# Kernel optimization log

Hardware: AMD Instinct MI355X
Metric: run time of the kernel (lower is better)

Reference implementation:

```python
import jax, jax.numpy as jnp
import numpy as np

NITERS = 5  # mean-field iterations (niters in __init__)


def setup_inputs() -> dict:
    key = jax.random.key(0)
    k1, k2 = jax.random.split(key)
    B, L, C, H, W = 2, 21, 3, 96, 96
    E0 = jax.random.normal(k1, (B, L, H, W), dtype=jnp.float32)
    Refs = jax.random.normal(k2, (B, C, H, W), dtype=jnp.float32)
    # potts_init: weight = ones(L,L) - eye(L)
    Mu_W = jnp.ones((L, L), dtype=jnp.float32) - jnp.eye(L, dtype=jnp.float32)
    return {"E0": E0, "Refs": Refs, "Mu_W": Mu_W}


def _affinity(Refs):
    # Reference-guided dense adjacency (BatchedAdjacency): row-normalized
    # Gaussian affinity on guide features, one N x N matrix per batch element.
    B, C, H, W = Refs.shape
    N = H * W
    f = Refs.reshape(B, C, N).transpose(0, 2, 1)  # [B, N, C]
    sq = jnp.sum(f * f, axis=-1)  # [B, N]
    D = sq[:, :, None] + sq[:, None, :] - 2.0 * jnp.einsum('bnc,bmc->bnm', f, f)
    A = jnp.exp(-0.5 * D)  # [B, N, N]
    return A / jnp.sum(A, axis=-1, keepdims=True)


def reference(E0, Refs, Mu_W):
    B, L, H, W = E0.shape
    N = H * W
    A = _affinity(Refs)  # computed once, reused every iteration
    E0f = E0.reshape(B, L, N)
    Qf = jax.nn.softmax(-E0f, axis=1)  # Q = softmax(-E0, dim=1)
    for _ in range(NITERS):
        # Potts compatibility transform (channel mixing): Mu(Q)
        M = jnp.einsum('kl,bln->bkn', Mu_W, Qf)
        # adjacency message passing: W(Mu(Q), Refs)
        msg = jnp.einsum('bnm,blm->bln', A, M)
        Qf = jax.nn.softmax(-(E0f + msg), axis=1)
    return Qf.reshape(B, L, H, W)
```

## Files before the change

### kernel.cpp

```cpp
#include <hip/hip_runtime.h>
#include <hip/hip_bf16.h>


#define BB 2
#define LL 21
#define LP (LL + 1)
#define NNPX 9216
#define NITERS 5
#define LOG2E 1.4426950408889634f

typedef __attribute__((ext_vector_type(8))) short short8;
typedef __attribute__((ext_vector_type(4))) float f32x4;

static __device__ inline unsigned int pk_bf16(float a, float b) {
    __hip_bfloat162 h = __float22bfloat162_rn(make_float2(a, b));
    unsigned int u;
    __builtin_memcpy(&u, &h, 4);
    return u;
}

__global__ __launch_bounds__(256) void k_prep(
        const float* __restrict__ E0, const float* __restrict__ Refs,
        const float* __restrict__ Mu,
        float4* __restrict__ FN, float4* __restrict__ FS,
        __hip_bfloat16* __restrict__ MQ) {
    __shared__ float muS[LL * LL];
    for (int i = threadIdx.x; i < LL * LL; i += 256) muS[i] = Mu[i];
    __syncthreads();

    int idx = blockIdx.x * 256 + threadIdx.x;
    int b = idx / NNPX, n = idx % NNPX;

    const float* rb = Refs + (size_t)b * 3 * NNPX + n;
    float r0 = rb[0], r1 = rb[NNPX], r2 = rb[2 * NNPX];
    FN[idx] = make_float4(r0, r1, r2, 0.f);
    float g = -0.5f * (r0 * r0 + r1 * r1 + r2 * r2);
    FS[idx] = make_float4(g * LOG2E, r0 * LOG2E, r1 * LOG2E, r2 * LOG2E);

    const float* eb = E0 + (size_t)b * LL * NNPX + n;
    float x[LL];
    float mx = -1e30f;
    for (int l = 0; l < LL; ++l) { x[l] = -eb[(size_t)l * NNPX]; mx = fmaxf(mx, x[l]); }
    float s = 0.f;
    for (int l = 0; l < LL; ++l) { x[l] = __builtin_amdgcn_exp2f((x[l] - mx) * LOG2E); s += x[l]; }
    float rs = __builtin_amdgcn_rcpf(s);
    for (int l = 0; l < LL; ++l) x[l] *= rs;

    __hip_bfloat16* mq = MQ + (size_t)b * LL * NNPX + n;
    for (int k = 0; k < LL; ++k) {
        float a = 0.f;
        for (int l = 0; l < LL; ++l) a += muS[k * LL + l] * x[l];
        mq[(size_t)k * NNPX] = __float2bfloat16(a);
    }
}

__global__ __launch_bounds__(256) void k_accum(
        const float4* __restrict__ FS, const float4* __restrict__ FN,
        const unsigned int* __restrict__ MQbf, float* __restrict__ Ppart, int S) {
    __shared__ __align__(16) unsigned short Wlds[64 * 72];
    __shared__ __align__(16) unsigned short Mlds[32 * 72];

    int t = threadIdx.x;
    int rb = blockIdx.x;
    int s  = blockIdx.y;
    int b  = rb / 144;
    int n0 = (rb % 144) * 64;
    int wv = t >> 6, lane = t & 63;

    for (int i = t; i < 32 * 72 / 2; i += 256) ((unsigned int*)Mlds)[i] = 0;
    if (t < 32) ((unsigned int*)&Mlds[21 * 72])[t] = 0x3F803F80u;

    int mq = t & 15;
    int ng = t >> 4;
    float4 fnr[4];
    for (int i = 0; i < 4; ++i) fnr[i] = FN[b * NNPX + n0 + ng + 16 * i];

    f32x4 acc0 = {0.f, 0.f, 0.f, 0.f};
    f32x4 acc1 = {0.f, 0.f, 0.f, 0.f};

    const unsigned int* mqb = MQbf + (size_t)b * LL * (NNPX / 2);

    for (int tile = s; tile < 144; tile += S) {
        int m0 = tile * 64;
        float4 fsr[4];
        for (int j = 0; j < 4; ++j) fsr[j] = FS[b * NNPX + m0 + 4 * mq + j];

        __syncthreads();

        for (int e = t; e < 21 * 32; e += 256) {
            int l = e >> 5, mo = e & 31;
            ((unsigned int*)&Mlds[l * 72])[mo] = mqb[(size_t)l * (NNPX / 2) + m0 / 2 + mo];
        }
        for (int i = 0; i < 4; ++i) {
            float4 f = fnr[i];
            float w0 = __builtin_amdgcn_exp2f(fsr[0].x + f.x * fsr[0].y + f.y * fsr[0].z + f.z * fsr[0].w);
            float w1 = __builtin_amdgcn_exp2f(fsr[1].x + f.x * fsr[1].y + f.y * fsr[1].z + f.z * fsr[1].w);
            float w2 = __builtin_amdgcn_exp2f(fsr[2].x + f.x * fsr[2].y + f.y * fsr[2].z + f.z * fsr[2].w);
            float w3 = __builtin_amdgcn_exp2f(fsr[3].x + f.x * fsr[3].y + f.y * fsr[3].z + f.z * fsr[3].w);
            uint2 pk;
            pk.x = pk_bf16(w0, w1);
            pk.y = pk_bf16(w2, w3);
            int n = ng + 16 * i;
            *(uint2*)&Wlds[n * 72 + 4 * mq] = pk;
        }
        __syncthreads();

        int row = wv * 16 + (lane & 15);
        int kof = (lane >> 4) * 8;
        short8 a0 = *(const short8*)&Wlds[row * 72 + kof];
        short8 a1 = *(const short8*)&Wlds[row * 72 + kof + 32];
        short8 b00 = *(const short8*)&Mlds[(lane & 15) * 72 + kof];
        short8 b01 = *(const short8*)&Mlds[(lane & 15) * 72 + kof + 32];
        short8 b10 = *(const short8*)&Mlds[(16 + (lane & 15)) * 72 + kof];
        short8 b11 = *(const short8*)&Mlds[(16 + (lane & 15)) * 72 + kof + 32];
        acc0 = __builtin_amdgcn_mfma_f32_16x16x32_bf16(a0, b00, acc0, 0, 0, 0);
        acc0 = __builtin_amdgcn_mfma_f32_16x16x32_bf16(a1, b01, acc0, 0, 0, 0);
        acc1 = __builtin_amdgcn_mfma_f32_16x16x32_bf16(a0, b10, acc1, 0, 0, 0);
        acc1 = __builtin_amdgcn_mfma_f32_16x16x32_bf16(a1, b11, acc1, 0, 0, 0);
    }

    int col = lane & 15, qr = lane >> 4;
    float* pp = Ppart + ((size_t)(s * BB + b) * LP) * NNPX;
    for (int r = 0; r < 4; ++r) {
        int n = n0 + wv * 16 + qr * 4 + r;
        pp[(size_t)col * NNPX + n] = acc0[r];
        if (col < LP - 16) pp[(size_t)(16 + col) * NNPX + n] = acc1[r];
    }
}

template <bool LAST>
__global__ __launch_bounds__(256) void k_softmax(
        const float* __restrict__ E0, const float* __restrict__ Ppart,
        const float* __restrict__ Mu,
        __hip_bfloat16* __restrict__ MQ, float* __restrict__ Out, int S) {
    __shared__ float muS[LL * LL];
    for (int i = threadIdx.x; i < LL * LL; i += 256) muS[i] = Mu[i];
    __syncthreads();

    int idx = blockIdx.x * 256 + threadIdx.x;
    int b = idx / NNPX, n = idx % NNPX;

    float P[LP];
    for (int l = 0; l < LP; ++l) P[l] = 0.f;
    for (int s = 0; s < S; ++s) {
        const float* pp = Ppart + ((size_t)(s * BB + b) * LP) * NNPX + n;
        for (int l = 0; l < LP; ++l) P[l] += pp[(size_t)l * NNPX];
    }
    float rinv = __builtin_amdgcn_rcpf(P[LL]);

    const float* eb = E0 + (size_t)b * LL * NNPX + n;
    float mx = -1e30f;
    for (int l = 0; l < LL; ++l) {
        P[l] = -(eb[(size_t)l * NNPX] + P[l] * rinv);
        mx = fmaxf(mx, P[l]);
    }
    float ssum = 0.f;
    for (int l = 0; l < LL; ++l) { P[l] = __builtin_amdgcn_exp2f((P[l] - mx) * LOG2E); ssum += P[l]; }
    float rs = __builtin_amdgcn_rcpf(ssum);
    for (int l = 0; l < LL; ++l) P[l] *= rs;

    if (LAST) {
        float* ob = Out + (size_t)b * LL * NNPX + n;
        for (int l = 0; l < LL; ++l) ob[(size_t)l * NNPX] = P[l];
    } else {
        __hip_bfloat16* mq = MQ + (size_t)b * LL * NNPX + n;
        for (int k = 0; k < LL; ++k) {
            float a = 0.f;
            for (int l = 0; l < LL; ++l) a += muS[k * LL + l] * P[l];
            mq[(size_t)k * NNPX] = __float2bfloat16(a);
        }
    }
}

extern "C" void kernel_launch(void* const* d_in, const int* in_sizes, int n_in,
                              void* d_out, int out_size, void* d_ws, size_t ws_size,
                              hipStream_t stream) {
    const float* E0   = (const float*)d_in[0];
    const float* Refs = (const float*)d_in[1];
    const float* Mu   = (const float*)d_in[2];
    float* out = (float*)d_out;

    char* w = (char*)d_ws;
    size_t off = 0;
    auto alloc = [&](size_t bytes) {
        void* p = w + off;
        off += (bytes + 255) & ~(size_t)255;
        return p;
    };
    float4* FN     = (float4*)alloc((size_t)BB * NNPX * sizeof(float4));
    float4* FS     = (float4*)alloc((size_t)BB * NNPX * sizeof(float4));
    __hip_bfloat16* MQbf = (__hip_bfloat16*)alloc((size_t)BB * LL * NNPX * sizeof(__hip_bfloat16));

    size_t per = (size_t)BB * LP * NNPX * sizeof(float);
    size_t avail = ws_size > off ? ws_size - off : 0;
    int Smax = (int)(avail / (per + 256));
    static const int divs[] = {8, 6, 4, 3, 2, 1};
    int S = 1;
    for (int i = 0; i < 6; ++i) if (divs[i] <= Smax) { S = divs[i]; break; }
    float* Ppart = (float*)alloc((size_t)S * per);

    k_prep<<<BB * NNPX / 256, 256, 0, stream>>>(E0, Refs, Mu, FN, FS, MQbf);
    for (int it = 0; it < NITERS; ++it) {
        k_accum<<<dim3(288, S), 256, 0, stream>>>(FS, FN, (const unsigned int*)MQbf, Ppart, S);
        if (it == NITERS - 1)
            k_softmax<true><<<BB * NNPX / 256, 256, 0, stream>>>(E0, Ppart, Mu, MQbf, out, S);
        else
            k_softmax<false><<<BB * NNPX / 256, 256, 0, stream>>>(E0, Ppart, Mu, MQbf, out, S);
    }
}
```

Baseline: 453.0 us.

## Build MFMA operands directly in registers, dropping LDS staging and barriers

The accumulation kernel no longer stages the affinity tile and the Mu(Q) tile through shared memory. Each lane now computes the exp2 affinity values for its own MFMA A-fragment in registers, packs them with v_cvt_pk_bf16_f32, and loads its B-fragments straight from global memory, with ones and zeros synthesized in registers for the padding rows. This removes both __syncthreads per tile and the LDS traffic, and adds an occupancy hint to launch_bounds. In exchange each lane issues more global loads of FS, with redundancy across lanes, and does some duplicated exp work.

```diff
diff --git a/kernel.cpp b/kernel.cpp
--- a/kernel.cpp
+++ b/kernel.cpp
@@ -11,13 +11,7 @@
 
 typedef __attribute__((ext_vector_type(8))) short short8;
 typedef __attribute__((ext_vector_type(4))) float f32x4;
-
-static __device__ inline unsigned int pk_bf16(float a, float b) {
-    __hip_bfloat162 h = __float22bfloat162_rn(make_float2(a, b));
-    unsigned int u;
-    __builtin_memcpy(&u, &h, 4);
-    return u;
-}
+typedef __attribute__((ext_vector_type(4))) unsigned int u32x4;
 
 __global__ __launch_bounds__(256) void k_prep(
         const float* __restrict__ E0, const float* __restrict__ Refs,
@@ -54,65 +48,91 @@
     }
 }
 
-__global__ __launch_bounds__(256) void k_accum(
+__global__ __launch_bounds__(256, 4) void k_accum(
         const float4* __restrict__ FS, const float4* __restrict__ FN,
-        const unsigned int* __restrict__ MQbf, float* __restrict__ Ppart, int S) {
-    __shared__ __align__(16) unsigned short Wlds[64 * 72];
-    __shared__ __align__(16) unsigned short Mlds[32 * 72];
-
+        const __hip_bfloat16* __restrict__ MQbf, float* __restrict__ Ppart, int S) {
     int t = threadIdx.x;
     int rb = blockIdx.x;
     int s  = blockIdx.y;
     int b  = rb / 144;
     int n0 = (rb % 144) * 64;
     int wv = t >> 6, lane = t & 63;
-
-    for (int i = t; i < 32 * 72 / 2; i += 256) ((unsigned int*)Mlds)[i] = 0;
-    if (t < 32) ((unsigned int*)&Mlds[21 * 72])[t] = 0x3F803F80u;
-
-    int mq = t & 15;
-    int ng = t >> 4;
-    float4 fnr[4];
-    for (int i = 0; i < 4; ++i) fnr[i] = FN[b * NNPX + n0 + ng + 16 * i];
+    int lr  = lane & 15;
+    int kof = (lane >> 4) * 8;
+
+    float4 fn = FN[b * NNPX + n0 + wv * 16 + lr];
 
     f32x4 acc0 = {0.f, 0.f, 0.f, 0.f};
     f32x4 acc1 = {0.f, 0.f, 0.f, 0.f};
 
-    const unsigned int* mqb = MQbf + (size_t)b * LL * (NNPX / 2);
+    const float4* fsb = FS + (size_t)b * NNPX;
+    const __hip_bfloat16* mqb = MQbf + (size_t)b * LL * NNPX;
+
+    const int l2 = 16 + lr;
+    short8 ones8;
+    {
+        u32x4 o = {0x3F803F80u, 0x3F803F80u, 0x3F803F80u, 0x3F803F80u};
+        ones8 = __builtin_bit_cast(short8, o);
+    }
+    short8 zero8;
+    {
+        u32x4 z = {0u, 0u, 0u, 0u};
+        zero8 = __builtin_bit_cast(short8, z);
+    }
 
     for (int tile = s; tile < 144; tile += S) {
         int m0 = tile * 64;
-        float4 fsr[4];
-        for (int j = 0; j < 4; ++j) fsr[j] = FS[b * NNPX + m0 + 4 * mq + j];
-
-        __syncthreads();
-
-        for (int e = t; e < 21 * 32; e += 256) {
-            int l = e >> 5, mo = e & 31;
-            ((unsigned int*)&Mlds[l * 72])[mo] = mqb[(size_t)l * (NNPX / 2) + m0 / 2 + mo];
-        }
-        for (int i = 0; i < 4; ++i) {
-            float4 f = fnr[i];
-            float w0 = __builtin_amdgcn_exp2f(fsr[0].x + f.x * fsr[0].y + f.y * fsr[0].z + f.z * fsr[0].w);
-            float w1 = __builtin_amdgcn_exp2f(fsr[1].x + f.x * fsr[1].y + f.y * fsr[1].z + f.z * fsr[1].w);
-            float w2 = __builtin_amdgcn_exp2f(fsr[2].x + f.x * fsr[2].y + f.y * fsr[2].z + f.z * fsr[2].w);
-            float w3 = __builtin_amdgcn_exp2f(fsr[3].x + f.x * fsr[3].y + f.y * fsr[3].z + f.z * fsr[3].w);
-            uint2 pk;
-            pk.x = pk_bf16(w0, w1);
-            pk.y = pk_bf16(w2, w3);
-            int n = ng + 16 * i;
-            *(uint2*)&Wlds[n * 72 + 4 * mq] = pk;
-        }
-        __syncthreads();
-
-        int row = wv * 16 + (lane & 15);
-        int kof = (lane >> 4) * 8;
-        short8 a0 = *(const short8*)&Wlds[row * 72 + kof];
-        short8 a1 = *(const short8*)&Wlds[row * 72 + kof + 32];
-        short8 b00 = *(const short8*)&Mlds[(lane & 15) * 72 + kof];
-        short8 b01 = *(const short8*)&Mlds[(lane & 15) * 72 + kof + 32];
-        short8 b10 = *(const short8*)&Mlds[(16 + (lane & 15)) * 72 + kof];
-        short8 b11 = *(const short8*)&Mlds[(16 + (lane & 15)) * 72 + kof + 32];
+
+        const __hip_bfloat16* r0 = mqb + (size_t)lr * NNPX + m0 + kof;
+        short8 b00 = *(const short8*)(r0);
+        short8 b01 = *(const short8*)(r0 + 32);
+        short8 b10, b11;
+        if (l2 < LL) {
+            const __hip_bfloat16* r1 = mqb + (size_t)l2 * NNPX + m0 + kof;
+            b10 = *(const short8*)(r1);
+            b11 = *(const short8*)(r1 + 32);
+        } else if (l2 == LL) {
+            b10 = ones8; b11 = ones8;
+        } else {
+            b10 = zero8; b11 = zero8;
+        }
+
+        float w0[8];
+        #pragma unroll
+        for (int j = 0; j < 8; ++j) {
+            float4 F = fsb[m0 + kof + j];
+            float lg = F.x + fn.x * F.y;
+            lg += fn.y * F.z;
+            lg += fn.z * F.w;
+            w0[j] = __builtin_amdgcn_exp2f(lg);
+        }
+        u32x4 ap0;
+        #pragma unroll
+        for (int j = 0; j < 4; ++j) {
+            unsigned int p;
+            asm("v_cvt_pk_bf16_f32 %0, %1, %2" : "=v"(p) : "v"(w0[2 * j]), "v"(w0[2 * j + 1]));
+            ap0[j] = p;
+        }
+        short8 a0 = __builtin_bit_cast(short8, ap0);
+
+        float w1[8];
+        #pragma unroll
+        for (int j = 0; j < 8; ++j) {
+            float4 F = fsb[m0 + 32 + kof + j];
+            float lg = F.x + fn.x * F.y;
+            lg += fn.y * F.z;
+            lg += fn.z * F.w;
+            w1[j] = __builtin_amdgcn_exp2f(lg);
+        }
+        u32x4 ap1;
+        #pragma unroll
+        for (int j = 0; j < 4; ++j) {
+            unsigned int p;
+            asm("v_cvt_pk_bf16_f32 %0, %1, %2" : "=v"(p) : "v"(w1[2 * j]), "v"(w1[2 * j + 1]));
+            ap1[j] = p;
+        }
+        short8 a1 = __builtin_bit_cast(short8, ap1);
+
         acc0 = __builtin_amdgcn_mfma_f32_16x16x32_bf16(a0, b00, acc0, 0, 0, 0);
         acc0 = __builtin_amdgcn_mfma_f32_16x16x32_bf16(a1, b01, acc0, 0, 0, 0);
         acc1 = __builtin_amdgcn_mfma_f32_16x16x32_bf16(a0, b10, acc1, 0, 0, 0);
@@ -201,7 +221,7 @@
 
     k_prep<<<BB * NNPX / 256, 256, 0, stream>>>(E0, Refs, Mu, FN, FS, MQbf);
     for (int it = 0; it < NITERS; ++it) {
-        k_accum<<<dim3(288, S), 256, 0, stream>>>(FS, FN, (const unsigned int*)MQbf, Ppart, S);
+        k_accum<<<dim3(288, S), 256, 0, stream>>>(FS, FN, MQbf, Ppart, S);
         if (it == NITERS - 1)
             k_softmax<true><<<BB * NNPX / 256, 256, 0, stream>>>(E0, Ppart, Mu, MQbf, out, S);
         else
```

New measurement: 761.7 us. +68.1%, slower.

## Double-buffer LDS tiles and prefetch next tile in accumulation kernel

Applied to the files above, without the earlier changes.

Restructures the k_accum tile loop into a double-buffered pipeline. Global loads for the next tile are issued before the MFMAs on the current tile, and the next tile's exp weights are written to the alternate LDS buffer afterwards, cutting the loop to one barrier per tile. The ones/zero padding rows of the M tile are now built in registers rather than stored in LDS, and launch bounds request 4 blocks per CU. Tiles are now split into contiguous chunks of 144/S, which assumes S divides 144. The extra LDS buffer and the register pressure from prefetching could limit occupancy.

```diff
diff --git a/kernel.cpp b/kernel.cpp
--- a/kernel.cpp
+++ b/kernel.cpp
@@ -11,6 +11,7 @@
 
 typedef __attribute__((ext_vector_type(8))) short short8;
 typedef __attribute__((ext_vector_type(4))) float f32x4;
+typedef __attribute__((ext_vector_type(4))) unsigned int u32x4;
 
 static __device__ inline unsigned int pk_bf16(float a, float b) {
     __hip_bfloat162 h = __float22bfloat162_rn(make_float2(a, b));
@@ -54,11 +55,11 @@
     }
 }
 
-__global__ __launch_bounds__(256) void k_accum(
+__global__ __launch_bounds__(256, 4) void k_accum(
         const float4* __restrict__ FS, const float4* __restrict__ FN,
         const unsigned int* __restrict__ MQbf, float* __restrict__ Ppart, int S) {
-    __shared__ __align__(16) unsigned short Wlds[64 * 72];
-    __shared__ __align__(16) unsigned short Mlds[32 * 72];
+    __shared__ __align__(16) unsigned short Wlds[2][64 * 72];
+    __shared__ __align__(16) unsigned short Mlds[2][21 * 72];
 
     int t = threadIdx.x;
     int rb = blockIdx.x;
@@ -66,31 +67,52 @@
     int b  = rb / 144;
     int n0 = (rb % 144) * 64;
     int wv = t >> 6, lane = t & 63;
-
-    for (int i = t; i < 32 * 72 / 2; i += 256) ((unsigned int*)Mlds)[i] = 0;
-    if (t < 32) ((unsigned int*)&Mlds[21 * 72])[t] = 0x3F803F80u;
+    int lr = lane & 15, g = lane >> 4;
 
     int mq = t & 15;
     int ng = t >> 4;
     float4 fnr[4];
     for (int i = 0; i < 4; ++i) fnr[i] = FN[b * NNPX + n0 + ng + 16 * i];
 
+    const int T  = 144 / S;
+    const int t0 = s * T;
+    const float4* fsb = FS + (size_t)b * NNPX;
+    const unsigned int* mqb = MQbf + (size_t)b * LL * (NNPX / 2);
+
+    int sl0 = t >> 5, sm0 = t & 31;
+    int sl1 = (t + 256) >> 5, sm1 = (t + 256) & 31;
+    int sl2 = (t + 512) >> 5, sm2 = (t + 512) & 31;
+
     f32x4 acc0 = {0.f, 0.f, 0.f, 0.f};
     f32x4 acc1 = {0.f, 0.f, 0.f, 0.f};
 
-    const unsigned int* mqb = MQbf + (size_t)b * LL * (NNPX / 2);
-
-    for (int tile = s; tile < 144; tile += S) {
-        int m0 = tile * 64;
-        float4 fsr[4];
-        for (int j = 0; j < 4; ++j) fsr[j] = FS[b * NNPX + m0 + 4 * mq + j];
-
-        __syncthreads();
-
-        for (int e = t; e < 21 * 32; e += 256) {
-            int l = e >> 5, mo = e & 31;
-            ((unsigned int*)&Mlds[l * 72])[mo] = mqb[(size_t)l * (NNPX / 2) + m0 / 2 + mo];
-        }
+    short8 ones8, zero8;
+    {
+        u32x4 o = {0x3F803F80u, 0x3F803F80u, 0x3F803F80u, 0x3F803F80u};
+        ones8 = __builtin_bit_cast(short8, o);
+        u32x4 z = {0u, 0u, 0u, 0u};
+        zero8 = __builtin_bit_cast(short8, z);
+    }
+
+    float4 fsr[4];
+    unsigned int mr0, mr1, mr2;
+
+    auto LOADFS = [&](int tile) {
+        int m0 = (t0 + tile) * 64;
+        #pragma unroll
+        for (int j = 0; j < 4; ++j) fsr[j] = fsb[m0 + 4 * mq + j];
+    };
+    auto LOADMQ = [&](int tile) {
+        int mo0 = (t0 + tile) * 32;
+        mr0 = mqb[(size_t)sl0 * (NNPX / 2) + mo0 + sm0];
+        mr1 = mqb[(size_t)sl1 * (NNPX / 2) + mo0 + sm1];
+        if (t < 160) mr2 = mqb[(size_t)sl2 * (NNPX / 2) + mo0 + sm2];
+    };
+    auto STORE = [&](int buf) {
+        ((unsigned int*)&Mlds[buf][sl0 * 72])[sm0] = mr0;
+        ((unsigned int*)&Mlds[buf][sl1 * 72])[sm1] = mr1;
+        if (t < 160) ((unsigned int*)&Mlds[buf][sl2 * 72])[sm2] = mr2;
+        #pragma unroll
         for (int i = 0; i < 4; ++i) {
             float4 f = fnr[i];
             float w0 = __builtin_amdgcn_exp2f(fsr[0].x + f.x * fsr[0].y + f.y * fsr[0].z + f.z * fsr[0].w);
@@ -100,23 +122,41 @@
             uint2 pk;
             pk.x = pk_bf16(w0, w1);
             pk.y = pk_bf16(w2, w3);
-            int n = ng + 16 * i;
-            *(uint2*)&Wlds[n * 72 + 4 * mq] = pk;
+            *(uint2*)&Wlds[buf][(ng + 16 * i) * 72 + 4 * mq] = pk;
         }
-        __syncthreads();
-
-        int row = wv * 16 + (lane & 15);
-        int kof = (lane >> 4) * 8;
-        short8 a0 = *(const short8*)&Wlds[row * 72 + kof];
-        short8 a1 = *(const short8*)&Wlds[row * 72 + kof + 32];
-        short8 b00 = *(const short8*)&Mlds[(lane & 15) * 72 + kof];
-        short8 b01 = *(const short8*)&Mlds[(lane & 15) * 72 + kof + 32];
-        short8 b10 = *(const short8*)&Mlds[(16 + (lane & 15)) * 72 + kof];
-        short8 b11 = *(const short8*)&Mlds[(16 + (lane & 15)) * 72 + kof + 32];
+    };
+
+    LOADFS(0);
+    LOADMQ(0);
+    STORE(0);
+    __syncthreads();
+
+    int row = wv * 16 + lr;
+    for (int tt = 0; tt < T; ++tt) {
+        int cur = tt & 1;
+        bool more = (tt + 1) < T;
+        if (more) { LOADFS(tt + 1); LOADMQ(tt + 1); }
+
+        short8 a0  = *(const short8*)&Wlds[cur][row * 72 + g * 8];
+        short8 a1  = *(const short8*)&Wlds[cur][row * 72 + g * 8 + 32];
+        short8 b00 = *(const short8*)&Mlds[cur][lr * 72 + g * 8];
+        short8 b01 = *(const short8*)&Mlds[cur][lr * 72 + g * 8 + 32];
+        short8 b10, b11;
+        if (lr < 5) {
+            b10 = *(const short8*)&Mlds[cur][(16 + lr) * 72 + g * 8];
+            b11 = *(const short8*)&Mlds[cur][(16 + lr) * 72 + g * 8 + 32];
+        } else if (lr == 5) {
+            b10 = ones8; b11 = ones8;
+        } else {
+            b10 = zero8; b11 = zero8;
+        }
         acc0 = __builtin_amdgcn_mfma_f32_16x16x32_bf16(a0, b00, acc0, 0, 0, 0);
         acc0 = __builtin_amdgcn_mfma_f32_16x16x32_bf16(a1, b01, acc0, 0, 0, 0);
         acc1 = __builtin_amdgcn_mfma_f32_16x16x32_bf16(a0, b10, acc1, 0, 0, 0);
         acc1 = __builtin_amdgcn_mfma_f32_16x16x32_bf16(a1, b11, acc1, 0, 0, 0);
+
+        if (more) STORE(cur ^ 1);
+        __syncthreads();
     }
 
     int col = lane & 15, qr = lane >> 4;
```

After: 398.1 us. -12.1%, faster.
